# Performance work log

Hardware: AMD Instinct MI355X
Metric: run time of the kernel (lower is better)

## Reference

```python
import jax, jax.numpy as jnp
import numpy as np

N = 100000          # nodes
E = 1600000         # edges (avg degree 16)
IN_DIM = 64
HID = 64
OUT = 32
NUM_GRAPHS = 64


def setup_inputs() -> dict:
    key = jax.random.key(0)
    ks = jax.random.split(key, 12)
    x = jax.random.normal(ks[0], (N, IN_DIM), dtype=jnp.float32)
    edge_index = jax.random.randint(ks[1], (2, E), 0, N, dtype=jnp.int64)
    batch = jnp.sort(jax.random.randint(ks[2], (N,), 0, NUM_GRAPHS, dtype=jnp.int64))
    s = 0.05
    return {
        "x": x,
        "edge_index": edge_index,
        "batch": batch,
        "w1_init": jax.random.normal(ks[3], (IN_DIM, HID), dtype=jnp.float32) * s,
        "w1_root": jax.random.normal(ks[4], (IN_DIM, HID), dtype=jnp.float32) * s,
        "b1": jnp.zeros((HID,), dtype=jnp.float32),
        "w2_init": jax.random.normal(ks[5], (HID, HID), dtype=jnp.float32) * s,
        "w2_root": jax.random.normal(ks[6], (HID, HID), dtype=jnp.float32) * s,
        "b2": jnp.zeros((HID,), dtype=jnp.float32),
        "fc_w": jax.random.normal(ks[7], (HID, OUT), dtype=jnp.float32) * s,
        "fc_b": jnp.zeros((OUT,), dtype=jnp.float32),
    }


def reference(x, edge_index, batch, w1_init, w1_root, b1, w2_init, w2_root, b2, fc_w, fc_b):
    row, col = edge_index[0], edge_index[1]
    # gcn_norm without self loops (ARMAConv default): deg over target nodes
    ones_e = jnp.ones((E,), dtype=x.dtype)
    deg = jax.ops.segment_sum(ones_e, col, num_segments=N)
    dinv = jnp.where(deg > 0, jax.lax.rsqrt(jnp.maximum(deg, 1.0)), 0.0)
    norm = dinv[row] * dinv[col]  # [E]

    def propagate(h):  # out[col] += norm * h[row]
        return jax.ops.segment_sum(h[row] * norm[:, None], col, num_segments=N)

    # ARMAConv (K=1, T=1, act=None): A_hat (x W_init) + x W_root + b
    h = jax.nn.relu(propagate(x @ w1_init) + x @ w1_root + b1)
    h = jax.nn.relu(propagate(h @ w2_init) + h @ w2_root + b2)

    # global mean pool over graphs
    cnt = jax.ops.segment_sum(jnp.ones((N,), dtype=h.dtype), batch, num_segments=NUM_GRAPHS)
    pooled = jax.ops.segment_sum(h, batch, num_segments=NUM_GRAPHS) / jnp.maximum(cnt, 1.0)[:, None]

    return pooled @ fc_w + fc_b  # [NUM_GRAPHS, OUT]
```

## Files before the change

### kernel.cpp

```cpp
#include <hip/hip_runtime.h>
#include <hip/hip_bf16.h>


#define NB 256
#define CAP 5120
#define MAXB 400
#define P1_CHUNK 2048

typedef unsigned int uint32;
typedef unsigned short ushort16;
typedef __attribute__((ext_vector_type(8))) short short8;
typedef __attribute__((ext_vector_type(4))) float f32x4;

__device__ inline uint32 bf16rn(float f) {
    uint32 u = __float_as_uint(f);
    uint32 r = ((u >> 16) & 1u) + 0x7FFFu;
    return (u + r) >> 16;
}
__device__ inline uint32 pack_bf16(float a, float b) {
    return bf16rn(a) | (bf16rn(b) << 16);
}
__device__ inline float bflo(uint32 u) { return __uint_as_float(u << 16); }
__device__ inline float bfhi(uint32 u) { return __uint_as_float(u & 0xFFFF0000u); }

__global__ __launch_bounds__(256) void bucket_kernel(
    const int* __restrict__ row, const int* __restrict__ col,
    uint32* __restrict__ bpack, int* __restrict__ bcnt, int E,
    const float* __restrict__ W1i, const float* __restrict__ W1r,
    const float* __restrict__ W2i, const float* __restrict__ W2r,
    ushort16* __restrict__ wt) {
    __shared__ int hist[MAXB];
    __shared__ int ofs[MAXB];
    __shared__ int cur[MAXB];
    __shared__ int gbase[MAXB];
    __shared__ int s[256];
    __shared__ uint32 stage[P1_CHUNK];
    __shared__ unsigned short stage_bk[P1_CHUNK];

    int t = threadIdx.x;

    if (blockIdx.x < 128) {
        int idx = blockIdx.x * 256 + t;
        int m = idx >> 12;
        int r = idx & 4095;
        int d = r >> 6, k = r & 63;
        const float* W = (m < 2) ? W1i : (m < 4) ? W1r : (m < 6) ? W2i : W2r;
        float v = W[k * 64 + d];
        uint32 hi = bf16rn(v);
        uint32 outv;
        if (m & 1) {
            float hf = __uint_as_float(hi << 16);
            outv = bf16rn(v - hf);
        } else {
            outv = hi;
        }
        wt[(size_t)m * 4096 + d * 64 + k] = (unsigned short)outv;
        return;
    }

    for (int i = t; i < MAXB; i += 256) hist[i] = 0;
    __syncthreads();

    int e0 = (blockIdx.x - 128) * P1_CHUNK;
    int cntE = min(E - e0, P1_CHUNK);

    for (int i = t; i < cntE; i += 256) {
        int c = col[e0 + i];
        atomicAdd(&hist[c >> 8], 1);
    }
    __syncthreads();

    int i2 = 2 * t;
    int a = (i2 < MAXB) ? hist[i2] : 0;
    int b = (i2 + 1 < MAXB) ? hist[i2 + 1] : 0;
    s[t] = a + b;
    __syncthreads();
    for (int off = 1; off < 256; off <<= 1) {
        int x = (t >= off) ? s[t - off] : 0;
        __syncthreads();
        s[t] += x;
        __syncthreads();
    }
    int excl = (t > 0) ? s[t - 1] : 0;
    if (i2 < MAXB) ofs[i2] = excl;
    if (i2 + 1 < MAXB) ofs[i2 + 1] = excl + a;
    __syncthreads();

    for (int i = t; i < MAXB; i += 256) {
        cur[i] = ofs[i];
        gbase[i] = hist[i] ? atomicAdd(&bcnt[i], hist[i]) : 0;
    }
    __syncthreads();

    for (int i = t; i < cntE; i += 256) {
        int c = col[e0 + i];
        int r = row[e0 + i];
        int bk = c >> 8;
        int k = atomicAdd(&cur[bk], 1);
        stage[k] = ((uint32)(c & 255) << 24) | (uint32)r;
        stage_bk[k] = (unsigned short)bk;
    }
    __syncthreads();

    for (int i = t; i < cntE; i += 256) {
        uint32 pk = stage[i];
        int bk = stage_bk[i];
        int gd = gbase[bk] + (i - ofs[bk]);
        if (gd < CAP) bpack[(size_t)bk * CAP + gd] = pk;
    }
}

__global__ __launch_bounds__(1024) void csr_kernel(
    const uint32* __restrict__ bpack, const int* __restrict__ bcnt,
    int* __restrict__ es, int* __restrict__ nstart, int* __restrict__ ndeg,
    float* __restrict__ dinv, int n) {
    __shared__ uint32 sbp[CAP];
    __shared__ int h[NB];
    __shared__ int s[NB];
    __shared__ int cur[NB];
    int b = blockIdx.x, t = threadIdx.x;
    if (t < NB) h[t] = 0;
    __syncthreads();
    int cnt = min(bcnt[b], CAP);
    size_t base = (size_t)b * CAP;
    for (int i = t; i < cnt; i += 1024) {
        uint32 pk = bpack[base + i];
        sbp[i] = pk;
        atomicAdd(&h[pk >> 24], 1);
    }
    __syncthreads();
    if (t < NB) s[t] = h[t];
    __syncthreads();
    for (int off = 1; off < NB; off <<= 1) {
        int x = 0;
        if (t < NB && t >= off) x = s[t - off];
        __syncthreads();
        if (t < NB) s[t] += x;
        __syncthreads();
    }
    if (t < NB) {
        int myofs = s[t] - h[t];
        cur[t] = myofs;
        int node = b * NB + t;
        if (node < n) {
            nstart[node] = (int)base + myofs;
            ndeg[node] = h[t];
            dinv[node] = h[t] ? rsqrtf((float)h[t]) : 0.0f;
        }
    }
    __syncthreads();
    for (int i = t; i < cnt; i += 1024) {
        uint32 pk = sbp[i];
        int cl = (int)(pk >> 24);
        int p = atomicAdd(&cur[cl], 1);
        es[base + p] = (int)(pk & 0xFFFFFFu);
    }
}

__global__ __launch_bounds__(256) void gemm_mfma(
    const void* __restrict__ Xin,
    const ushort16* __restrict__ wt4,
    const float* __restrict__ bias, const float* __restrict__ dinv,
    ushort16* __restrict__ Ts, ushort16* __restrict__ Rs, int n, int xf32) {
    __shared__ unsigned short sXs[64 * 72];
    int t = threadIdx.x;
    int node0 = blockIdx.x * 64;

    if (xf32) {
        const float* X = (const float*)Xin;
        for (int i = t; i < 1024; i += 256) {
            int r = i >> 4, c4 = (i & 15) * 4;
            int node = node0 + r;
            float4 v = make_float4(0.f, 0.f, 0.f, 0.f);
            if (node < n) v = *(const float4*)&X[(size_t)node * 64 + c4];
            *(uint32*)&sXs[r * 72 + c4] = pack_bf16(v.x, v.y);
            *(uint32*)&sXs[r * 72 + c4 + 2] = pack_bf16(v.z, v.w);
        }
    } else {
        const uint32* Xb2 = (const uint32*)Xin;
        for (int i = t; i < 512; i += 256) {
            int r = i >> 3, kg = i & 7;
            int node = node0 + r;
            uint4 v = make_uint4(0u, 0u, 0u, 0u);
            if (node < n) v = *(const uint4*)&Xb2[(size_t)node * 32 + kg * 4];
            *(uint4*)&sXs[r * 72 + kg * 8] = v;
        }
    }

    int w = t >> 6;
    int lane = t & 63;
    int q = lane >> 4;
    int col = lane & 15;
    int dim = w * 16 + col;

    short8 bih[2], bil[2], brh[2], brl[2];
#pragma unroll
    for (int kh = 0; kh < 2; ++kh) {
        size_t o = (size_t)dim * 64 + kh * 32 + q * 8;
        bih[kh] = *(const short8*)&wt4[0 * 4096 + o];
        bil[kh] = *(const short8*)&wt4[1 * 4096 + o];
        brh[kh] = *(const short8*)&wt4[2 * 4096 + o];
        brl[kh] = *(const short8*)&wt4[3 * 4096 + o];
    }
    float4 bias4 = *(const float4*)&bias[w * 16 + q * 4];
    __syncthreads();

    unsigned short* TsU = (unsigned short*)Ts;
    unsigned short* RsU = (unsigned short*)Rs;

#pragma unroll
    for (int mt = 0; mt < 4; ++mt) {
        int rbase = mt * 16 + col;
        short8 a0 = *(const short8*)&sXs[rbase * 72 + q * 8];
        short8 a1 = *(const short8*)&sXs[rbase * 72 + 32 + q * 8];
        f32x4 accT = {0.f, 0.f, 0.f, 0.f};
        f32x4 accR = {0.f, 0.f, 0.f, 0.f};
        accT = __builtin_amdgcn_mfma_f32_16x16x32_bf16(bih[0], a0, accT, 0, 0, 0);
        accT = __builtin_amdgcn_mfma_f32_16x16x32_bf16(bih[1], a1, accT, 0, 0, 0);
        accT = __builtin_amdgcn_mfma_f32_16x16x32_bf16(bil[0], a0, accT, 0, 0, 0);
        accT = __builtin_amdgcn_mfma_f32_16x16x32_bf16(bil[1], a1, accT, 0, 0, 0);
        accR = __builtin_amdgcn_mfma_f32_16x16x32_bf16(brh[0], a0, accR, 0, 0, 0);
        accR = __builtin_amdgcn_mfma_f32_16x16x32_bf16(brh[1], a1, accR, 0, 0, 0);
        accR = __builtin_amdgcn_mfma_f32_16x16x32_bf16(brl[0], a0, accR, 0, 0, 0);
        accR = __builtin_amdgcn_mfma_f32_16x16x32_bf16(brl[1], a1, accR, 0, 0, 0);

        int node = node0 + mt * 16 + col;
        if (node < n) {
            float dv = dinv[node];
            uint2 pT, pR;
            pT.x = pack_bf16(accT[0] * dv, accT[1] * dv);
            pT.y = pack_bf16(accT[2] * dv, accT[3] * dv);
            pR.x = pack_bf16(accR[0] + bias4.x, accR[1] + bias4.y);
            pR.y = pack_bf16(accR[2] + bias4.z, accR[3] + bias4.w);
            size_t o = (size_t)node * 64 + w * 16 + q * 4;
            *(uint2*)&TsU[o] = pT;
            *(uint2*)&RsU[o] = pR;
        }
    }
}

__global__ __launch_bounds__(256) void gather_fused(
    const uint2* __restrict__ Ts2, const uint2* __restrict__ Rs2,
    const int* __restrict__ es, const int* __restrict__ nstart,
    const int* __restrict__ ndeg, const float* __restrict__ dinv,
    uint2* __restrict__ Hb2, int n) {
    int c = blockIdx.x * 4 + (threadIdx.x >> 6);
    if (c >= n) return;
    int lane = threadIdx.x & 63;
    int q = lane >> 4;
    int d4 = lane & 15;
    int deg = ndeg[c];
    int s0 = nstart[c];
    float a0 = 0.f, a1 = 0.f, a2 = 0.f, a3 = 0.f;
    for (int base = 0; base < deg; base += 64) {
        int m = min(deg - base, 64);
        int sid = (lane < m) ? __builtin_nontemporal_load(&es[s0 + base + lane]) : 0;
        for (int j = 0; j < m; j += 16) {
            int e0 = j + q, e1 = j + 4 + q, e2 = j + 8 + q, e3 = j + 12 + q;
            int r0 = __shfl(sid, e0);
            int r1 = __shfl(sid, e1);
            int r2 = __shfl(sid, e2);
            int r3 = __shfl(sid, e3);
            uint2 z = make_uint2(0u, 0u);
            uint2 v0 = (e0 < m) ? Ts2[(size_t)r0 * 16 + d4] : z;
            uint2 v1 = (e1 < m) ? Ts2[(size_t)r1 * 16 + d4] : z;
            uint2 v2 = (e2 < m) ? Ts2[(size_t)r2 * 16 + d4] : z;
            uint2 v3 = (e3 < m) ? Ts2[(size_t)r3 * 16 + d4] : z;
            a0 += bflo(v0.x) + bflo(v1.x) + bflo(v2.x) + bflo(v3.x);
            a1 += bfhi(v0.x) + bfhi(v1.x) + bfhi(v2.x) + bfhi(v3.x);
            a2 += bflo(v0.y) + bflo(v1.y) + bflo(v2.y) + bflo(v3.y);
            a3 += bfhi(v0.y) + bfhi(v1.y) + bfhi(v2.y) + bfhi(v3.y);
        }
    }
    a0 += __shfl_xor(a0, 16); a0 += __shfl_xor(a0, 32);
    a1 += __shfl_xor(a1, 16); a1 += __shfl_xor(a1, 32);
    a2 += __shfl_xor(a2, 16); a2 += __shfl_xor(a2, 32);
    a3 += __shfl_xor(a3, 16); a3 += __shfl_xor(a3, 32);
    if (lane < 16) {
        float dc = dinv[c];
        uint2 ur = Rs2[(size_t)c * 16 + d4];
        float h0 = fmaxf(fmaf(dc, a0, bflo(ur.x)), 0.0f);
        float h1 = fmaxf(fmaf(dc, a1, bfhi(ur.x)), 0.0f);
        float h2 = fmaxf(fmaf(dc, a2, bflo(ur.y)), 0.0f);
        float h3 = fmaxf(fmaf(dc, a3, bfhi(ur.y)), 0.0f);
        Hb2[(size_t)c * 16 + d4] = make_uint2(pack_bf16(h0, h1), pack_bf16(h2, h3));
    }
}

__global__ __launch_bounds__(256) void pool_kernel(
    const uint32* __restrict__ Hb, const int* __restrict__ batch,
    float* __restrict__ pooled, float* __restrict__ cnt, int n) {
    __shared__ float sAcc[64 * 64];
    __shared__ float sCnt[64];
    int tid = threadIdx.x;
    for (int i = tid; i < 4096; i += 256) sAcc[i] = 0.0f;
    if (tid < 64) sCnt[tid] = 0.0f;
    __syncthreads();

    int w = tid >> 6, lane = tid & 63;
    int half = lane >> 5, d2 = lane & 31;
    int s = blockIdx.x * 256 + w * 64;
    int e = min(s + 64, n);
    float a0 = 0.0f, a1 = 0.0f, c = 0.0f;
    int gcur = -1;
    for (int i = s + half; i < e; i += 2) {
        int g = batch[i];
        if (g != gcur) {
            if (gcur >= 0) {
                atomicAdd(&sAcc[gcur * 64 + 2 * d2], a0);
                atomicAdd(&sAcc[gcur * 64 + 2 * d2 + 1], a1);
                if (d2 == 0) atomicAdd(&sCnt[gcur], c);
            }
            gcur = g; a0 = 0.0f; a1 = 0.0f; c = 0.0f;
        }
        uint32 u = Hb[(size_t)i * 32 + d2];
        a0 += bflo(u);
        a1 += bfhi(u);
        c += 1.0f;
    }
    if (gcur >= 0) {
        atomicAdd(&sAcc[gcur * 64 + 2 * d2], a0);
        atomicAdd(&sAcc[gcur * 64 + 2 * d2 + 1], a1);
        if (d2 == 0) atomicAdd(&sCnt[gcur], c);
    }
    __syncthreads();
    for (int i = tid; i < 4096; i += 256) {
        float v = sAcc[i];
        if (v != 0.0f) atomicAdd(&pooled[i], v);
    }
    if (tid < 64) {
        float v = sCnt[tid];
        if (v != 0.0f) atomicAdd(&cnt[tid], v);
    }
}

__global__ void final_fc(const float* __restrict__ pooled, const float* __restrict__ cnt,
                         const float* __restrict__ fcw, const float* __restrict__ fcb,
                         float* __restrict__ out) {
    int idx = blockIdx.x * 256 + threadIdx.x;
    if (idx >= 64 * 32) return;
    int g = idx >> 5, o = idx & 31;
    float c = fmaxf(cnt[g], 1.0f);
    float acc = 0.0f;
#pragma unroll
    for (int k = 0; k < 64; ++k) acc = fmaf(pooled[g * 64 + k], fcw[k * 32 + o], acc);
    out[idx] = acc / c + fcb[o];
}

extern "C" void kernel_launch(void* const* d_in, const int* in_sizes, int n_in,
                              void* d_out, int out_size, void* d_ws, size_t ws_size,
                              hipStream_t stream) {
    const float* x       = (const float*)d_in[0];
    const int*   eidx    = (const int*)d_in[1];
    const int*   batch   = (const int*)d_in[2];
    const float* w1_init = (const float*)d_in[3];
    const float* w1_root = (const float*)d_in[4];
    const float* b1      = (const float*)d_in[5];
    const float* w2_init = (const float*)d_in[6];
    const float* w2_root = (const float*)d_in[7];
    const float* b2      = (const float*)d_in[8];
    const float* fc_w    = (const float*)d_in[9];
    const float* fc_b    = (const float*)d_in[10];
    float* out = (float*)d_out;

    const int N = in_sizes[0] / 64;
    const int E = in_sizes[1] / 2;
    const int* row = eidx;
    const int* col = eidx + E;

    const int B = (N + NB - 1) / NB;

    uint32* bpack = (uint32*)d_ws;
    int*   es     = (int*)(bpack + (size_t)B * CAP);
    int*   bcnt   = es + (size_t)B * CAP;
    float* pooled = (float*)(bcnt + MAXB);
    float* cnt    = pooled + 64 * 64;
    int*   nstart = (int*)(cnt + 64);
    int*   ndeg   = nstart + N;
    float* dinv   = (float*)(ndeg + N);
    uint32* wtU   = (uint32*)(dinv + N);
    uint32* Ts    = wtU + 16384;
    uint32* Rs    = Ts + (size_t)N * 32;
    uint32* Hb    = Rs + (size_t)N * 32;
    ushort16* wt  = (ushort16*)wtU;

    hipMemsetAsync(bcnt, 0, (size_t)(MAXB + 64 * 64 + 64) * sizeof(int), stream);

    const int EB = (E + P1_CHUNK - 1) / P1_CHUNK;
    bucket_kernel<<<128 + EB, 256, 0, stream>>>(row, col, bpack, bcnt, E,
                                                w1_init, w1_root, w2_init, w2_root, wt);
    csr_kernel<<<B, 1024, 0, stream>>>(bpack, bcnt, es, nstart, ndeg, dinv, N);

    gemm_mfma<<<(N + 63) / 64, 256, 0, stream>>>(x, wt, b1, dinv,
                                                 (ushort16*)Ts, (ushort16*)Rs, N, 1);
    gather_fused<<<(N + 3) / 4, 256, 0, stream>>>((const uint2*)Ts, (const uint2*)Rs,
                                                  es, nstart, ndeg, dinv, (uint2*)Hb, N);

    gemm_mfma<<<(N + 63) / 64, 256, 0, stream>>>(Hb, wt + (size_t)4 * 4096, b2, dinv,
                                                 (ushort16*)Ts, (ushort16*)Rs, N, 0);
    gather_fused<<<(N + 3) / 4, 256, 0, stream>>>((const uint2*)Ts, (const uint2*)Rs,
                                                  es, nstart, ndeg, dinv, (uint2*)Hb, N);

    pool_kernel<<<(N + 255) / 256, 256, 0, stream>>>(Hb, batch, pooled, cnt, N);
    final_fc<<<(64 * 32 + 255) / 256, 256, 0, stream>>>(pooled, cnt, fc_w, fc_b, out);
}
```

Baseline: 294.5 us.

## Load GEMM operands directly into registers and fuse final FC into pool kernel

The GEMM kernel drops its shared-memory staging of X and the block barrier, and each lane now loads its MFMA A-fragment straight from global memory (converting fp32 to bf16 in registers for layer 1). The final FC kernel is folded into the pool kernel through a last-block-done atomic counter, which removes one launch. The gather kernel's edge-index load is also changed from a nontemporal load to a regular cached load. Risks: the per-lane global reads are less coalesced than the old staged loads, and the last-block pattern depends on fences and a counter that is zeroed by the existing memset.

```diff
diff --git a/kernel.cpp b/kernel.cpp
--- a/kernel.cpp
+++ b/kernel.cpp
@@ -22,6 +22,12 @@
 }
 __device__ inline float bflo(uint32 u) { return __uint_as_float(u << 16); }
 __device__ inline float bfhi(uint32 u) { return __uint_as_float(u & 0xFFFF0000u); }
+
+union frag_u {
+    uint4 u4;
+    short8 s8;
+    uint32 u[4];
+};
 
 __global__ __launch_bounds__(256) void bucket_kernel(
     const int* __restrict__ row, const int* __restrict__ col,
@@ -162,30 +168,8 @@
     const ushort16* __restrict__ wt4,
     const float* __restrict__ bias, const float* __restrict__ dinv,
     ushort16* __restrict__ Ts, ushort16* __restrict__ Rs, int n, int xf32) {
-    __shared__ unsigned short sXs[64 * 72];
     int t = threadIdx.x;
     int node0 = blockIdx.x * 64;
-
-    if (xf32) {
-        const float* X = (const float*)Xin;
-        for (int i = t; i < 1024; i += 256) {
-            int r = i >> 4, c4 = (i & 15) * 4;
-            int node = node0 + r;
-            float4 v = make_float4(0.f, 0.f, 0.f, 0.f);
-            if (node < n) v = *(const float4*)&X[(size_t)node * 64 + c4];
-            *(uint32*)&sXs[r * 72 + c4] = pack_bf16(v.x, v.y);
-            *(uint32*)&sXs[r * 72 + c4 + 2] = pack_bf16(v.z, v.w);
-        }
-    } else {
-        const uint32* Xb2 = (const uint32*)Xin;
-        for (int i = t; i < 512; i += 256) {
-            int r = i >> 3, kg = i & 7;
-            int node = node0 + r;
-            uint4 v = make_uint4(0u, 0u, 0u, 0u);
-            if (node < n) v = *(const uint4*)&Xb2[(size_t)node * 32 + kg * 4];
-            *(uint4*)&sXs[r * 72 + kg * 8] = v;
-        }
-    }
 
     int w = t >> 6;
     int lane = t & 63;
@@ -203,28 +187,52 @@
         brl[kh] = *(const short8*)&wt4[3 * 4096 + o];
     }
     float4 bias4 = *(const float4*)&bias[w * 16 + q * 4];
-    __syncthreads();
 
     unsigned short* TsU = (unsigned short*)Ts;
     unsigned short* RsU = (unsigned short*)Rs;
 
 #pragma unroll
     for (int mt = 0; mt < 4; ++mt) {
-        int rbase = mt * 16 + col;
-        short8 a0 = *(const short8*)&sXs[rbase * 72 + q * 8];
-        short8 a1 = *(const short8*)&sXs[rbase * 72 + 32 + q * 8];
+        int node = node0 + mt * 16 + col;
+        frag_u a0, a1;
+        if (xf32) {
+            float4 f0 = make_float4(0.f, 0.f, 0.f, 0.f), f1 = f0, f2 = f0, f3 = f0;
+            if (node < n) {
+                const float* Xr = (const float*)Xin + (size_t)node * 64 + q * 8;
+                f0 = *(const float4*)(Xr);
+                f1 = *(const float4*)(Xr + 4);
+                f2 = *(const float4*)(Xr + 32);
+                f3 = *(const float4*)(Xr + 36);
+            }
+            a0.u[0] = pack_bf16(f0.x, f0.y);
+            a0.u[1] = pack_bf16(f0.z, f0.w);
+            a0.u[2] = pack_bf16(f1.x, f1.y);
+            a0.u[3] = pack_bf16(f1.z, f1.w);
+            a1.u[0] = pack_bf16(f2.x, f2.y);
+            a1.u[1] = pack_bf16(f2.z, f2.w);
+            a1.u[2] = pack_bf16(f3.x, f3.y);
+            a1.u[3] = pack_bf16(f3.z, f3.w);
+        } else {
+            a0.u4 = make_uint4(0u, 0u, 0u, 0u);
+            a1.u4 = make_uint4(0u, 0u, 0u, 0u);
+            if (node < n) {
+                const uint32* Xr = (const uint32*)Xin + (size_t)node * 32 + q * 4;
+                a0.u4 = *(const uint4*)(Xr);
+                a1.u4 = *(const uint4*)(Xr + 16);
+            }
+        }
+
         f32x4 accT = {0.f, 0.f, 0.f, 0.f};
         f32x4 accR = {0.f, 0.f, 0.f, 0.f};
-        accT = __builtin_amdgcn_mfma_f32_16x16x32_bf16(bih[0], a0, accT, 0, 0, 0);
-        accT = __builtin_amdgcn_mfma_f32_16x16x32_bf16(bih[1], a1, accT, 0, 0, 0);
-        accT = __builtin_amdgcn_mfma_f32_16x16x32_bf16(bil[0], a0, accT, 0, 0, 0);
-        accT = __builtin_amdgcn_mfma_f32_16x16x32_bf16(bil[1], a1, accT, 0, 0, 0);
-        accR = __builtin_amdgcn_mfma_f32_16x16x32_bf16(brh[0], a0, accR, 0, 0, 0);
-        accR = __builtin_amdgcn_mfma_f32_16x16x32_bf16(brh[1], a1, accR, 0, 0, 0);
-        accR = __builtin_amdgcn_mfma_f32_16x16x32_bf16(brl[0], a0, accR, 0, 0, 0);
-        accR = __builtin_amdgcn_mfma_f32_16x16x32_bf16(brl[1], a1, accR, 0, 0, 0);
-
-        int node = node0 + mt * 16 + col;
+        accT = __builtin_amdgcn_mfma_f32_16x16x32_bf16(bih[0], a0.s8, accT, 0, 0, 0);
+        accT = __builtin_amdgcn_mfma_f32_16x16x32_bf16(bih[1], a1.s8, accT, 0, 0, 0);
+        accT = __builtin_amdgcn_mfma_f32_16x16x32_bf16(bil[0], a0.s8, accT, 0, 0, 0);
+        accT = __builtin_amdgcn_mfma_f32_16x16x32_bf16(bil[1], a1.s8, accT, 0, 0, 0);
+        accR = __builtin_amdgcn_mfma_f32_16x16x32_bf16(brh[0], a0.s8, accR, 0, 0, 0);
+        accR = __builtin_amdgcn_mfma_f32_16x16x32_bf16(brh[1], a1.s8, accR, 0, 0, 0);
+        accR = __builtin_amdgcn_mfma_f32_16x16x32_bf16(brl[0], a0.s8, accR, 0, 0, 0);
+        accR = __builtin_amdgcn_mfma_f32_16x16x32_bf16(brl[1], a1.s8, accR, 0, 0, 0);
+
         if (node < n) {
             float dv = dinv[node];
             uint2 pT, pR;
@@ -254,7 +262,7 @@
     float a0 = 0.f, a1 = 0.f, a2 = 0.f, a3 = 0.f;
     for (int base = 0; base < deg; base += 64) {
         int m = min(deg - base, 64);
-        int sid = (lane < m) ? __builtin_nontemporal_load(&es[s0 + base + lane]) : 0;
+        int sid = (lane < m) ? es[s0 + base + lane] : 0;
         for (int j = 0; j < m; j += 16) {
             int e0 = j + q, e1 = j + 4 + q, e2 = j + 8 + q, e3 = j + 12 + q;
             int r0 = __shfl(sid, e0);
@@ -289,9 +297,12 @@
 
 __global__ __launch_bounds__(256) void pool_kernel(
     const uint32* __restrict__ Hb, const int* __restrict__ batch,
-    float* __restrict__ pooled, float* __restrict__ cnt, int n) {
+    float* __restrict__ pooled, float* __restrict__ cnt, int n,
+    const float* __restrict__ fcw, const float* __restrict__ fcb,
+    float* __restrict__ out, int* __restrict__ done, int nblocks) {
     __shared__ float sAcc[64 * 64];
     __shared__ float sCnt[64];
+    __shared__ int isLast;
     int tid = threadIdx.x;
     for (int i = tid; i < 4096; i += 256) sAcc[i] = 0.0f;
     if (tid < 64) sCnt[tid] = 0.0f;
@@ -332,19 +343,31 @@
         float v = sCnt[tid];
         if (v != 0.0f) atomicAdd(&cnt[tid], v);
     }
-}
-
-__global__ void final_fc(const float* __restrict__ pooled, const float* __restrict__ cnt,
-                         const float* __restrict__ fcw, const float* __restrict__ fcb,
-                         float* __restrict__ out) {
-    int idx = blockIdx.x * 256 + threadIdx.x;
-    if (idx >= 64 * 32) return;
-    int g = idx >> 5, o = idx & 31;
-    float c = fmaxf(cnt[g], 1.0f);
-    float acc = 0.0f;
+
+    __threadfence();
+    __syncthreads();
+    if (tid == 0) {
+        int v = atomicAdd(done, 1);
+        isLast = (v == nblocks - 1);
+    }
+    __syncthreads();
+    if (!isLast) return;
+    __threadfence();
+    float pc[64];
+    float pl[64];
+    for (int idx = tid; idx < 64 * 32; idx += 256) {
+        int g = idx >> 5, o = idx & 31;
+        float cg = __hip_atomic_load(&cnt[g], __ATOMIC_RELAXED, __HIP_MEMORY_SCOPE_AGENT);
+        cg = fmaxf(cg, 1.0f);
+        float acc = 0.0f;
 #pragma unroll
-    for (int k = 0; k < 64; ++k) acc = fmaf(pooled[g * 64 + k], fcw[k * 32 + o], acc);
-    out[idx] = acc / c + fcb[o];
+        for (int k = 0; k < 64; ++k) {
+            float pv = __hip_atomic_load(&pooled[g * 64 + k], __ATOMIC_RELAXED, __HIP_MEMORY_SCOPE_AGENT);
+            acc = fmaf(pv, fcw[k * 32 + o], acc);
+        }
+        out[idx] = acc / cg + fcb[o];
+    }
+    (void)pc; (void)pl;
 }
 
 extern "C" void kernel_launch(void* const* d_in, const int* in_sizes, int n_in,
@@ -375,7 +398,8 @@
     int*   bcnt   = es + (size_t)B * CAP;
     float* pooled = (float*)(bcnt + MAXB);
     float* cnt    = pooled + 64 * 64;
-    int*   nstart = (int*)(cnt + 64);
+    int*   done   = (int*)(cnt + 64);
+    int*   nstart = done + 16;
     int*   ndeg   = nstart + N;
     float* dinv   = (float*)(ndeg + N);
     uint32* wtU   = (uint32*)(dinv + N);
@@ -384,10 +408,10 @@
     uint32* Hb    = Rs + (size_t)N * 32;
     ushort16* wt  = (ushort16*)wtU;
 
-    hipMemsetAsync(bcnt, 0, (size_t)(MAXB + 64 * 64 + 64) * sizeof(int), stream);
+    hipMemsetAsync(bcnt, 0, (size_t)(MAXB + 64 * 64 + 64 + 16) * sizeof(int), stream);
 
     const int EB = (E + P1_CHUNK - 1) / P1_CHUNK;
-    bucket_kernel<<<128 + EB, 256, 0, stream>>>(row, col, bpack, bcnt, E,
+    bucket_kernel<<<128 + EB, 256, 0, stream>>>(row, col, bpack, (int*)bcnt, E,
                                                 w1_init, w1_root, w2_init, w2_root, wt);
     csr_kernel<<<B, 1024, 0, stream>>>(bpack, bcnt, es, nstart, ndeg, dinv, N);
 
@@ -401,6 +425,7 @@
     gather_fused<<<(N + 3) / 4, 256, 0, stream>>>((const uint2*)Ts, (const uint2*)Rs,
                                                   es, nstart, ndeg, dinv, (uint2*)Hb, N);
 
-    pool_kernel<<<(N + 255) / 256, 256, 0, stream>>>(Hb, batch, pooled, cnt, N);
-    final_fc<<<(64 * 32 + 255) / 256, 256, 0, stream>>>(pooled, cnt, fc_w, fc_b, out);
-}
+    const int PB = (N + 255) / 256;
+    pool_kernel<<<PB, 256, 0, stream>>>(Hb, batch, pooled, cnt, N,
+                                        fc_w, fc_b, out, done, PB);
+}
```

After: 330.4 us. +12.2%, slower.
